# Kernel optimization log

Measured on AMD Instinct MI355X. Metric: run time of the kernel, lower is better.

Reference implementation:

```python
import jax, jax.numpy as jnp
import numpy as np

C_P = 1004.0
R_EARTH = 6371000.0
R_GAS = 287.0
OMEGA_E = 7.292e-05
B, K, H, W = 1, 8, 361, 720
KK = 5   # kernel basis size
D = 5    # neighborhood width in lat and lon (radius 2)
NS = K * 4 + 1
FCH = K * 4
NU = 2.0e5  # diffusion coefficient


def _ch(k, kind):
    return k * 4 + kind


def disco_gather(x, psi, quad):
    # DISCO sparse neighborhood aggregation on the sphere.
    # x: (B,C,H,W); psi: (KK,2,H,D,D) lat-dependent filter basis (2 directional comps)
    # returns (B,C,KK,2,H,W)
    Bx, C, Hx, Wx = x.shape
    Kk, nc, _, Dlat, Dlon = psi.shape
    r = Dlat // 2
    lat = np.clip(np.arange(Hx)[:, None] + np.arange(Dlat)[None, :] - r, 0, Hx - 1)
    out = jnp.zeros((Bx, C, Kk, nc, Hx, Wx), x.dtype)
    for dl in range(Dlat):
        li = lat[:, dl]
        xg = x[:, :, li, :] * quad[li][None, None, :, None]  # quadrature-weighted gather
        for dw in range(Dlon):
            xs = jnp.roll(xg, -(dw - r), axis=-1)  # circular in longitude
            out = out + psi[:, :, :, dl, dw][None, None, :, :, :, None] * xs[:, :, None, None, :, :]
    return out


def setup_inputs():
    key = jax.random.key(0)
    k1, k2, k3 = jax.random.split(key, 3)
    uv = jax.random.normal(k1, (B, K, H, W, 2), jnp.float32)
    T = jax.random.normal(k2, (B, K, H, W), jnp.float32)
    q = jax.random.normal(k3, (B, K, H, W), jnp.float32)
    rng = np.random.RandomState(0)
    psi = ((rng.rand(KK, 2, H, D, D) - 0.5) / (D * D)).astype(np.float32)
    colat = np.linspace(0.0, np.pi, H)
    quad = (np.sin(colat) * np.pi / (H - 1)).astype(np.float32)
    f_cor = (2.0 * OMEGA_E * np.sin(np.pi / 2.0 - colat)).astype(np.float32)
    p = np.array([1e5 * np.exp(-k * np.log(10.0) / (K - 1)) for k in range(K)], np.float32)
    lpr = np.log(p[:-1] / p[1:])
    p_low = np.concatenate([p[:1], 0.5 * (p[:-1] + p[1:])])
    p_up = np.concatenate([0.5 * (p[:-1] + p[1:]), [0.0]])
    dp = (p_low - p_up).astype(np.float32)
    # physics-encoded weights (module freezes all params and sets them analytically)
    W_ss_blk = np.zeros((NS, NS, KK), np.float32)
    W_vs_blk = np.zeros((NS, K, KK, 2), np.float32)
    for k in range(K):
        W_vs_blk[_ch(k, 2), k, :, 0] = 1.0 / R_EARTH  # zeta (curl)
        W_vs_blk[_ch(k, 3), k, :, 1] = 1.0 / R_EARTH  # div
    W_sv_blk = np.zeros((K, NS, KK, 2), np.float32)
    for ko in range(K):
        for ki in range(ko):
            W_sv_blk[ko, _ch(ki, 0), :, 1] = -R_GAS * lpr[ki] / R_EARTH  # PGF
        W_sv_blk[ko, _ch(ko, 1), :, 1] = -1.0 / R_EARTH  # -grad KE
    W_vv_blk = np.zeros((K, K, KK, 2), np.float32)
    W_vs2_blk = np.zeros((NS, K, KK, 2), np.float32)
    W_pw_ss = np.zeros((NS, NS), np.float32)
    W_pw_ss[FCH, FCH] = 1.0
    W_svp = np.zeros((NS, K, 2), np.float32)
    for k in range(K):
        W_svp[_ch(k, 2), k, 1] = 1.0
    W_svp[FCH, :, 1] = -1.0
    W_pw_vv = np.zeros((K, K), np.float32)
    W_ss_adv = np.zeros((2 * K, 2 * K, KK), np.float32)
    W_vs_adv = np.zeros((2 * K, K, KK, 2), np.float32)
    W_vs2_adv = np.zeros((2 * K, K, KK, 2), np.float32)
    for k in range(K):
        W_vs2_adv[k, k, :, 1] = -1.0 / R_EARTH      # -V.grad T
        W_vs2_adv[K + k, k, :, 1] = -1.0 / R_EARTH  # -V.grad q
    W_sv_grad = np.zeros((1, 1, KK, 2), np.float32)
    W_sv_grad[0, 0, :, 1] = 1.0 / R_EARTH
    W_vs_div = np.zeros((1, 1, KK, 2), np.float32)
    W_vs_div[0, 0, :, 1] = 1.0 / R_EARTH
    j = jnp.asarray
    return dict(uv=uv, T=T, q=q, psi=j(psi), quad=j(quad), f_cor=j(f_cor), p_levels=j(p), delta_p=j(dp),
                W_ss_blk=j(W_ss_blk), W_vs_blk=j(W_vs_blk), W_sv_blk=j(W_sv_blk), W_vv_blk=j(W_vv_blk),
                W_vs2_blk=j(W_vs2_blk), W_pw_ss=j(W_pw_ss), W_svp=j(W_svp), W_pw_vv=j(W_pw_vv),
                W_ss_adv=j(W_ss_adv), W_vs_adv=j(W_vs_adv), W_vs2_adv=j(W_vs2_adv),
                W_sv_grad=j(W_sv_grad), W_vs_div=j(W_vs_div))


def _forward(uv, T, q, psi, quad, f_cor, p_levels, delta_p, W_ss_blk, W_vs_blk, W_sv_blk, W_vv_blk,
             W_vs2_blk, W_pw_ss, W_svp, W_pw_vv, W_ss_adv, W_vs_adv, W_vs2_adv, W_sv_grad, W_vs_div):
    Bx, Kx, Hx, Wx = T.shape
    ke = 0.5 * (uv[..., 0] ** 2 + uv[..., 1] ** 2)
    zeros = jnp.zeros_like(T)
    per = jnp.stack([T, ke, zeros, zeros], axis=2).reshape(Bx, Kx * 4, Hx, Wx)
    f_field = jnp.broadcast_to(f_cor[None, None, :, None], (Bx, 1, Hx, Wx))
    x_s = jnp.concatenate([per, f_field], axis=1)  # (B, 4K+1, H, W)
    # ---- Block 1: VectorDiscoBlock ----
    Gs = disco_gather(x_s, psi, quad)               # (B,NS,KK,2,H,W)
    Ga = disco_gather(uv[..., 0], psi, quad)
    Gb = disco_gather(uv[..., 1], psi, quad)
    Gdir = jnp.stack([Ga[:, :, :, 0], Gb[:, :, :, 1]], axis=3)  # curl/div pairing
    Giso = jnp.stack([Ga[:, :, :, 0], Gb[:, :, :, 0]], axis=3)
    ys_c = jnp.einsum('oik,bikhw->bohw', W_ss_blk, Gs[:, :, :, 0])
    ys_c = ys_c + jnp.einsum('oikc,bikchw->bohw', W_vs_blk, Gdir)
    ys_c = ys_c + jnp.einsum('oikc,bokchw,bihwc->bohw', W_vs2_blk, Gs, uv)
    yv_c = jnp.einsum('oikc,bikchw->bohwc', W_sv_blk, Gs)
    yv_c = yv_c + jnp.einsum('oikc,bikchw->bohwc', W_vv_blk, Giso)
    s_feat = ys_c + jnp.einsum('oi,bihw->bohw', W_pw_ss, x_s)
    coef0 = jnp.einsum('ij,bihw->bjhw', W_svp[:, :, 0], s_feat)
    coef1 = jnp.einsum('ij,bihw->bjhw', W_svp[:, :, 1], s_feat)
    cross = jnp.stack([-uv[..., 1], uv[..., 0]], axis=-1)  # k-hat x V
    sv = coef0[..., None] * uv + coef1[..., None] * cross
    y_v = uv + yv_c + sv + jnp.einsum('oi,bihwc->bohwc', W_pw_vv, uv)
    y_s = s_feat
    duv_dt = y_v - uv
    # omega from divergence (upward pressure integral)
    div = y_s[:, :Kx * 4].reshape(Bx, Kx, 4, Hx, Wx)[:, :, 3]
    cum = jnp.cumsum(div * delta_p[None, :, None, None], axis=1)
    omega = 0.5 * (jnp.concatenate([jnp.zeros_like(cum[:, :1]), cum[:, :-1]], axis=1) + cum)
    # ---- adv_conv (W_vs2 pathway): -V.grad(T), -V.grad(q) ----
    tq = jnp.concatenate([T, q], axis=1)
    Gtq = disco_gather(tq, psi, quad)
    dTq = jnp.einsum('oik,bikhw->bohw', W_ss_adv, Gtq[:, :, :, 0])
    dTq = dTq + jnp.einsum('oikc,bikchw->bohw', W_vs_adv, Gdir)
    dTq = dTq + jnp.einsum('oikc,bokchw,bihwc->bohw', W_vs2_adv, Gtq, uv)
    dT_dt = dTq[:, :Kx]
    dq_dt = dTq[:, Kx:]
    # dT/dp central differences
    p = p_levels
    inter = (T[:, 2:] - T[:, :-2]) / (p[2:] - p[:-2])[None, :, None, None]
    first = (T[:, 1:2] - T[:, 0:1]) / (p[1] - p[0])
    last = (T[:, -1:] - T[:, -2:-1]) / (p[-1] - p[-2])
    dTdp = jnp.concatenate([first, inter, last], axis=1)
    pk = p[None, :, None, None]
    dT_dt = dT_dt + omega * (R_GAS / C_P * T / pk - dTdp)
    # ---- diffusion: nu * div(grad(s)) via grad_conv/div_conv ----
    def lap(s):
        sf = s.reshape(Bx * Kx, 1, Hx, Wx)
        Gsf = disco_gather(sf, psi, quad)
        g = jnp.einsum('oikc,bikchw->bohwc', W_sv_grad, Gsf)  # (BK,1,H,W,2)
        Gga = disco_gather(g[..., 0], psi, quad)
        Ggb = disco_gather(g[..., 1], psi, quad)
        Gd = jnp.stack([Gga[:, :, :, 0], Ggb[:, :, :, 1]], axis=3)
        return jnp.einsum('oikc,bikchw->bohw', W_vs_div, Gd).reshape(Bx, Kx, Hx, Wx)
    dT_dt = dT_dt + NU * lap(T)
    dq_dt = dq_dt + NU * lap(q)
    duv_dt = duv_dt + NU * jnp.stack([lap(uv[..., 0]), lap(uv[..., 1])], axis=-1)
    return duv_dt, dT_dt, dq_dt


def reference(uv, T, q, psi, quad, f_cor, p_levels, delta_p, W_ss_blk, W_vs_blk, W_sv_blk, W_vv_blk,
              W_vs2_blk, W_pw_ss, W_svp, W_pw_vv, W_ss_adv, W_vs_adv, W_vs2_adv, W_sv_grad, W_vs_div):
    return _forward(uv, T, q, psi, quad, f_cor, p_levels, delta_p, W_ss_blk, W_vs_blk, W_sv_blk,
                    W_vv_blk, W_vs2_blk, W_pw_ss, W_svp, W_pw_vv, W_ss_adv, W_vs_adv, W_vs2_adv,
                    W_sv_grad, W_vs_div)
```

## Files before the change

### kernel.cpp

```cpp
#include <hip/hip_runtime.h>


constexpr int Kz = 8, Hh = 361, Ww = 720;
constexpr int HW = Hh * Ww;
constexpr int OFF_DT = Kz * HW * 2;
constexpr int OFF_DQ = OFF_DT + Kz * HW;

constexpr int TH = 16, TW = 64;
constexpr int SH = TH + 8, SW4 = TW + 8;
constexpr int EH = TH + 4, EW4 = TW + 4;
constexpr int SW4P = 73;
constexpr int EW4P = 69;

__device__ __forceinline__ int clipH(int x) {
  return x < 0 ? 0 : (x > Hh - 1 ? Hh - 1 : x);
}

#define FMA4(acc, s, v)                                                        \
  do {                                                                         \
    acc.x = fmaf((s), (v).x, acc.x);                                           \
    acc.y = fmaf((s), (v).y, acc.y);                                           \
    acc.z = fmaf((s), (v).z, acc.z);                                           \
    acc.w = fmaf((s), (v).w, acc.w);                                           \
  } while (0)

#define ROWV(acc, a, b, c, d, e)                                               \
  do {                                                                         \
    FMA4(acc, wq0, a); FMA4(acc, wq1, b); FMA4(acc, wq2, c);                   \
    FMA4(acc, wq3, d); FMA4(acc, wq4, e);                                      \
  } while (0)

#define ROW5S(acc, q0, q1, q2, q3, q4, a, b, c, d, e)                          \
  acc = fmaf(q0, a, fmaf(q1, b, fmaf(q2, c, fmaf(q3, d, fmaf(q4, e, acc)))))

__global__ __launch_bounds__(256, 2) void pe_pass1(
    const float2* __restrict__ uv,
    const float*  __restrict__ Tg,
    const float*  __restrict__ qg,
    const float*  __restrict__ psi,
    const float*  __restrict__ quad,
    const float*  __restrict__ f_cor,
    const float*  __restrict__ delta_p,
    float* __restrict__ out,
    float2* __restrict__ ws)
{
  __shared__ float4 S4[SH][SW4P];
  __shared__ float4 d1S[EH][EW4P];
  __shared__ __align__(16) float uSh[SH][SW4];
  __shared__ __align__(16) float keSh[SH][SW4];
  __shared__ float P1L[EH][25];
  __shared__ float P0L[TH][25];
  __shared__ float quadA[SH];

  const int tid = threadIdx.x;
  const int tx = tid & 15;
  const int ty = tid >> 4;
  const int w0 = blockIdx.x * TW;
  const int h0 = blockIdx.y * TH;
  const int k  = blockIdx.z;

  if (tid < SH) quadA[tid] = quad[clipH(h0 + tid - 4)];
  for (int idx = tid; idx < EH * 25; idx += 256) {
    int ee = idx / 25, t = idx - ee * 25;
    int p = clipH(h0 + ee - 2);
    float s = 0.f;
    #pragma unroll
    for (int kk = 0; kk < 5; ++kk)
      s += psi[kk * (2 * Hh * 25) + Hh * 25 + p * 25 + t];
    P1L[ee][t] = s;
  }
  for (int idx = tid; idx < TH * 25; idx += 256) {
    int r = idx / 25, t = idx - r * 25;
    int p = clipH(h0 + r);
    float s = 0.f;
    #pragma unroll
    for (int kk = 0; kk < 5; ++kk)
      s += psi[kk * (2 * Hh * 25) + p * 25 + t];
    P0L[r][t] = s;
  }

  for (int idx = tid; idx < SH * SW4; idx += 256) {
    int rr = idx / SW4, cc = idx - rr * SW4;
    int pr = clipH(h0 + rr - 4);
    int pc = w0 + cc - 4;
    pc = pc < 0 ? pc + Ww : (pc >= Ww ? pc - Ww : pc);
    int g = (k * Hh + pr) * Ww + pc;
    float2 uvv = uv[g];
    float tv = Tg[g], qv_ = qg[g];
    S4[rr][cc] = make_float4(uvv.x, uvv.y, tv, qv_);
    if (cc >= 2) {
      uSh[rr][cc - 2]  = uvv.x;
      keSh[rr][cc - 2] = 0.5f * (uvv.x * uvv.x + uvv.y * uvv.y);
    }
  }
  __syncthreads();

  for (int idx = tid; idx < EH * (EW4 / 4); idx += 256) {
    int ee = idx / (EW4 / 4), gc = idx - ee * (EW4 / 4);
    int cb = gc * 4;
    int p = clipH(h0 + ee - 2);
    float4 a0 = {0,0,0,0}, a1 = {0,0,0,0}, a2 = {0,0,0,0}, a3 = {0,0,0,0};
    #pragma unroll
    for (int dl = 0; dl < 5; ++dl) {
      int sp = clipH(p + dl - 2);
      int rr = sp - h0 + 4;
      float qv = quadA[rr];
      const float4* row = &S4[rr][cb];
      float4 g0 = row[0], g1 = row[1], g2 = row[2], g3 = row[3];
      float4 g4 = row[4], g5 = row[5], g6 = row[6], g7 = row[7];
      const float* wr = &P1L[ee][dl * 5];
      float wq0 = qv * wr[0], wq1 = qv * wr[1], wq2 = qv * wr[2];
      float wq3 = qv * wr[3], wq4 = qv * wr[4];
      ROWV(a0, g0, g1, g2, g3, g4);
      ROWV(a1, g1, g2, g3, g4, g5);
      ROWV(a2, g2, g3, g4, g5, g6);
      ROWV(a3, g3, g4, g5, g6, g7);
    }
    d1S[ee][cb + 0] = a0; d1S[ee][cb + 1] = a1;
    d1S[ee][cb + 2] = a2; d1S[ee][cb + 3] = a3;
  }
  __syncthreads();

  const int h = h0 + ty;
  const int hc = h < Hh ? h : (Hh - 1);
  const int wbase = w0 + tx * 4;
  const float f = f_cor[hc];
  const float invR = (float)(1.0 / 6371000.0);
  const float cL = 200000.0f * invR * invR;

  float4 lp0 = {0,0,0,0}, lp1 = {0,0,0,0}, lp2 = {0,0,0,0}, lp3 = {0,0,0,0};
  float du0 = 0.f, du1 = 0.f, du2 = 0.f, du3 = 0.f;
  float dk0 = 0.f, dk1 = 0.f, dk2 = 0.f, dk3 = 0.f;
  #pragma unroll
  for (int dl = 0; dl < 5; ++dl) {
    int sp = clipH(hc + dl - 2);
    int er = sp - h0 + 2;
    int rr = er + 2;
    float qv = quadA[rr];
    {
      const float4* row = &d1S[er][tx * 4];
      float4 g0 = row[0], g1 = row[1], g2 = row[2], g3 = row[3];
      float4 g4 = row[4], g5 = row[5], g6 = row[6], g7 = row[7];
      const float* wr = &P1L[ty + 2][dl * 5];
      float wq0 = qv * wr[0], wq1 = qv * wr[1], wq2 = qv * wr[2];
      float wq3 = qv * wr[3], wq4 = qv * wr[4];
      ROWV(lp0, g0, g1, g2, g3, g4);
      ROWV(lp1, g1, g2, g3, g4, g5);
      ROWV(lp2, g2, g3, g4, g5, g6);
      ROWV(lp3, g3, g4, g5, g6, g7);
    }
    {
      float4 A = *(const float4*)&uSh[rr][tx * 4];
      float4 B = *(const float4*)&uSh[rr][tx * 4 + 4];
      const float* w0r = &P0L[ty][dl * 5];
      float q0 = qv * w0r[0], q1 = qv * w0r[1], q2 = qv * w0r[2];
      float q3 = qv * w0r[3], q4 = qv * w0r[4];
      ROW5S(du0, q0, q1, q2, q3, q4, A.x, A.y, A.z, A.w, B.x);
      ROW5S(du1, q0, q1, q2, q3, q4, A.y, A.z, A.w, B.x, B.y);
      ROW5S(du2, q0, q1, q2, q3, q4, A.z, A.w, B.x, B.y, B.z);
      ROW5S(du3, q0, q1, q2, q3, q4, A.w, B.x, B.y, B.z, B.w);
    }
    {
      float4 A = *(const float4*)&keSh[rr][tx * 4];
      float4 B = *(const float4*)&keSh[rr][tx * 4 + 4];
      const float* w1r = &P1L[ty + 2][dl * 5];
      float q0 = qv * w1r[0], q1 = qv * w1r[1], q2 = qv * w1r[2];
      float q3 = qv * w1r[3], q4 = qv * w1r[4];
      ROW5S(dk0, q0, q1, q2, q3, q4, A.x, A.y, A.z, A.w, B.x);
      ROW5S(dk1, q0, q1, q2, q3, q4, A.y, A.z, A.w, B.x, B.y);
      ROW5S(dk2, q0, q1, q2, q3, q4, A.z, A.w, B.x, B.y, B.z);
      ROW5S(dk3, q0, q1, q2, q3, q4, A.w, B.x, B.y, B.z, B.w);
    }
  }

  if (h < Hh && wbase < Ww) {
    const float dpk = delta_p[k];
    float4 duvA, duvB, dTv, dqv, wsA, wsB;
    {
      float4 d1c = d1S[ty + 2][tx * 4 + 2];
      float4 ctr = S4[ty + 4][tx * 4 + 4];
      float coef1 = fmaf(du0, invR, -f);
      duvA.x = fmaf(-coef1, ctr.y, cL * lp0.x);
      duvA.y = fmaf(coef1, ctr.x, -invR * dk0) + cL * lp0.y;
      dTv.x = -(invR * d1c.z) * ctr.y + cL * lp0.z;
      dqv.x = fmaf(-(invR * d1c.w), ctr.y, cL * lp0.w);
      wsA.x = invR * d1c.y * dpk; wsA.y = d1c.z;
    }
    {
      float4 d1c = d1S[ty + 2][tx * 4 + 3];
      float4 ctr = S4[ty + 4][tx * 4 + 5];
      float coef1 = fmaf(du1, invR, -f);
      duvA.z = fmaf(-coef1, ctr.y, cL * lp1.x);
      duvA.w = fmaf(coef1, ctr.x, -invR * dk1) + cL * lp1.y;
      dTv.y = -(invR * d1c.z) * ctr.y + cL * lp1.z;
      dqv.y = fmaf(-(invR * d1c.w), ctr.y, cL * lp1.w);
      wsA.z = invR * d1c.y * dpk; wsA.w = d1c.z;
    }
    {
      float4 d1c = d1S[ty + 2][tx * 4 + 4];
      float4 ctr = S4[ty + 4][tx * 4 + 6];
      float coef1 = fmaf(du2, invR, -f);
      duvB.x = fmaf(-coef1, ctr.y, cL * lp2.x);
      duvB.y = fmaf(coef1, ctr.x, -invR * dk2) + cL * lp2.y;
      dTv.z = -(invR * d1c.z) * ctr.y + cL * lp2.z;
      dqv.z = fmaf(-(invR * d1c.w), ctr.y, cL * lp2.w);
      wsB.x = invR * d1c.y * dpk; wsB.y = d1c.z;
    }
    {
      float4 d1c = d1S[ty + 2][tx * 4 + 5];
      float4 ctr = S4[ty + 4][tx * 4 + 7];
      float coef1 = fmaf(du3, invR, -f);
      duvB.z = fmaf(-coef1, ctr.y, cL * lp3.x);
      duvB.w = fmaf(coef1, ctr.x, -invR * dk3) + cL * lp3.y;
      dTv.w = -(invR * d1c.z) * ctr.y + cL * lp3.z;
      dqv.w = fmaf(-(invR * d1c.w), ctr.y, cL * lp3.w);
      wsB.z = invR * d1c.y * dpk; wsB.w = d1c.z;
    }
    const int gidx = (k * Hh + h) * Ww + wbase;
    float4* o4 = (float4*)out;
    o4[gidx >> 1] = duvA;
    o4[(gidx >> 1) + 1] = duvB;
    *(float4*)&out[OFF_DT + gidx] = dTv;
    *(float4*)&out[OFF_DQ + gidx] = dqv;
    float4* w4 = (float4*)ws;
    w4[gidx >> 1] = wsA;
    w4[(gidx >> 1) + 1] = wsB;
  }
}

__global__ __launch_bounds__(256) void pe_pass2(
    const float* __restrict__ Tg,
    const float* __restrict__ p_levels,
    const float2* __restrict__ ws,
    float* __restrict__ out)
{
  int hw = blockIdx.x * 256 + threadIdx.x;
  if (hw >= HW) return;
  const float invR = (float)(1.0 / 6371000.0);
  const float RCP = (float)(287.0 / 1004.0);

  float pl[Kz];
  #pragma unroll
  for (int k = 0; k < Kz; ++k) pl[k] = p_levels[k];

  float cum = 0.f, sumT = 0.f;
  float Tm = 0.f, Tc = Tg[hw];
  float2* o2 = (float2*)out;

  #pragma unroll
  for (int k = 0; k < Kz; ++k) {
    float Tp = (k < Kz - 1) ? Tg[(k + 1) * HW + hw] : 0.f;
    float2 wsv = ws[k * HW + hw];
    float omega = fmaf(0.5f, wsv.x, cum);
    cum += wsv.x;

    float dTdp;
    if (k == 0)            dTdp = (Tp - Tc) / (pl[1] - pl[0]);
    else if (k == Kz - 1)  dTdp = (Tc - Tm) / (pl[Kz - 1] - pl[Kz - 2]);
    else                   dTdp = (Tp - Tm) / (pl[k + 1] - pl[k - 1]);

    float fac = (RCP * Tc) / pl[k] - dTdp;
    out[OFF_DT + k * HW + hw] += omega * fac;

    float2 o = o2[k * HW + hw];
    o.y += sumT;
    o2[k * HW + hw] = o;

    if (k < Kz - 1) {
      float lpr = logf(pl[k] / pl[k + 1]);
      sumT = fmaf(-287.0f * lpr * invR, wsv.y, sumT);
    }
    Tm = Tc; Tc = Tp;
  }
}

constexpr int FTH = 16, FTW = 16;
constexpr int FSH = FTH + 8, FSW = FTW + 8;
constexpr int FEH = FTH + 4, FEW = FTW + 4;
constexpr int FSWp = FSW + 1, FEWp = FEW + 1;

__global__ __launch_bounds__(256) void pe_step(
    const float2* __restrict__ uv,
    const float*  __restrict__ Tg,
    const float*  __restrict__ qg,
    const float*  __restrict__ psi,
    const float*  __restrict__ quad,
    const float*  __restrict__ f_cor,
    const float*  __restrict__ p_levels,
    const float*  __restrict__ delta_p,
    float* __restrict__ out)
{
  __shared__ float uS[FSH][FSWp], vS[FSH][FSWp], TS[FSH][FSWp], qS[FSH][FSWp];
  __shared__ float keS[FEH][FEWp];
  __shared__ float d1uS[FEH][FEWp], d1vS[FEH][FEWp], d1TS[FEH][FEWp], d1qS[FEH][FEWp];
  __shared__ float P1L[FEH][25];
  __shared__ float P0L[FTH][25];
  __shared__ float quadA[FSH];
  __shared__ float pl[8], dps[8];

  const int tid = threadIdx.x;
  const int tx = tid & (FTW - 1);
  const int ty = tid >> 4;
  const int w0 = blockIdx.x * FTW;
  const int h0 = blockIdx.y * FTH;

  if (tid < FSH) quadA[tid] = quad[clipH(h0 + tid - 4)];
  if (tid < 8) { pl[tid] = p_levels[tid]; dps[tid] = delta_p[tid]; }
  for (int idx = tid; idx < FEH * 25; idx += 256) {
    int ee = idx / 25, t = idx - ee * 25;
    int p = clipH(h0 + ee - 2);
    float s = 0.f;
    #pragma unroll
    for (int kk = 0; kk < 5; ++kk)
      s += psi[kk * (2 * Hh * 25) + Hh * 25 + p * 25 + t];
    P1L[ee][t] = s;
  }
  for (int idx = tid; idx < FTH * 25; idx += 256) {
    int r = idx / 25, t = idx - r * 25;
    int p = clipH(h0 + r);
    float s = 0.f;
    #pragma unroll
    for (int kk = 0; kk < 5; ++kk)
      s += psi[kk * (2 * Hh * 25) + p * 25 + t];
    P0L[r][t] = s;
  }
  __syncthreads();

  const int h = h0 + ty;
  const bool act = h < Hh;
  const int hc = act ? h : (Hh - 1);
  const int w = w0 + tx;
  const float f = f_cor[hc];
  const float invR = (float)(1.0 / 6371000.0);
  const float cL = 200000.0f * invR * invR;
  const float RCP = (float)(287.0 / 1004.0);

  float cum = 0.f;
  float sumT = 0.f;

  #pragma unroll 1
  for (int k = 0; k < Kz; ++k) {
    __syncthreads();
    for (int idx = tid; idx < FSH * FSW; idx += 256) {
      int rr = idx / FSW, cc = idx - rr * FSW;
      int pr = clipH(h0 + rr - 4);
      int pc = w0 + cc - 4;
      pc = pc < 0 ? pc + Ww : (pc >= Ww ? pc - Ww : pc);
      int g = (k * Hh + pr) * Ww + pc;
      float2 uvv = uv[g];
      uS[rr][cc] = uvv.x; vS[rr][cc] = uvv.y;
      TS[rr][cc] = Tg[g]; qS[rr][cc] = qg[g];
    }
    __syncthreads();
    for (int idx = tid; idx < FEH * FEW; idx += 256) {
      int ee = idx / FEW, ec = idx - ee * FEW;
      float su = uS[ee + 2][ec + 2], sv = vS[ee + 2][ec + 2];
      keS[ee][ec] = 0.5f * (su * su + sv * sv);
    }
    for (int idx = tid; idx < FEH * FEW; idx += 256) {
      int ee = idx / FEW, ec = idx - ee * FEW;
      int p = clipH(h0 + ee - 2);
      float au = 0.f, av = 0.f, aT = 0.f, aq = 0.f;
      #pragma unroll
      for (int dl = 0; dl < 5; ++dl) {
        int sp = clipH(p + dl - 2);
        int rr = sp - h0 + 4;
        float qv = quadA[rr];
        float ru = 0.f, rv = 0.f, rT = 0.f, rq = 0.f;
        #pragma unroll
        for (int dw = 0; dw < 5; ++dw) {
          float wgt = P1L[ee][dl * 5 + dw];
          ru = fmaf(wgt, uS[rr][ec + dw], ru);
          rv = fmaf(wgt, vS[rr][ec + dw], rv);
          rT = fmaf(wgt, TS[rr][ec + dw], rT);
          rq = fmaf(wgt, qS[rr][ec + dw], rq);
        }
        au = fmaf(qv, ru, au); av = fmaf(qv, rv, av);
        aT = fmaf(qv, rT, aT); aq = fmaf(qv, rq, aq);
      }
      d1uS[ee][ec] = au; d1vS[ee][ec] = av;
      d1TS[ee][ec] = aT; d1qS[ee][ec] = aq;
    }
    __syncthreads();

    float d0u = 0.f, d1ke = 0.f;
    #pragma unroll
    for (int dl = 0; dl < 5; ++dl) {
      int sp = clipH(hc + dl - 2);
      int rr = sp - h0 + 4;
      int er = sp - h0 + 2;
      float qv = quadA[rr];
      float r0 = 0.f, rk = 0.f;
      #pragma unroll
      for (int dw = 0; dw < 5; ++dw) {
        r0 = fmaf(P0L[ty][dl * 5 + dw], uS[rr][tx + 2 + dw], r0);
        rk = fmaf(P1L[ty + 2][dl * 5 + dw], keS[er][tx + dw], rk);
      }
      d0u = fmaf(qv, r0, d0u);
      d1ke = fmaf(qv, rk, d1ke);
    }

    float lapu = 0.f, lapv = 0.f, lapT = 0.f, lapq = 0.f;
    #pragma unroll
    for (int dl = 0; dl < 5; ++dl) {
      int sp = clipH(hc + dl - 2);
      int er = sp - h0 + 2;
      float qv = quadA[er + 2];
      float ru = 0.f, rv = 0.f, rT = 0.f, rq = 0.f;
      #pragma unroll
      for (int dw = 0; dw < 5; ++dw) {
        float wgt = P1L[ty + 2][dl * 5 + dw];
        ru = fmaf(wgt, d1uS[er][tx + dw], ru);
        rv = fmaf(wgt, d1vS[er][tx + dw], rv);
        rT = fmaf(wgt, d1TS[er][tx + dw], rT);
        rq = fmaf(wgt, d1qS[er][tx + dw], rq);
      }
      lapu = fmaf(qv, ru, lapu); lapv = fmaf(qv, rv, lapv);
      lapT = fmaf(qv, rT, lapT); lapq = fmaf(qv, rq, lapq);
    }

    float d1T_c = d1TS[ty + 2][tx + 2];
    float d1v_c = d1vS[ty + 2][tx + 2];
    float d1q_c = d1qS[ty + 2][tx + 2];
    float uc = uS[ty + 4][tx + 4], vc = vS[ty + 4][tx + 4];
    float Tc = TS[ty + 4][tx + 4];

    float coef1 = fmaf(d0u, invR, -f);
    float duv0 = fmaf(-coef1, vc, cL * lapu);
    float yv1 = fmaf(-invR, d1ke, sumT);
    float duv1 = fmaf(coef1, uc, yv1) + cL * lapv;

    float div = invR * d1v_c;
    float dpk = dps[k];
    float omega = fmaf(0.5f * div, dpk, cum);
    cum = fmaf(div, dpk, cum);

    int gidx = (k * Hh + hc) * Ww + w;
    float dTdp;
    if (k == 0) {
      float Tp = Tg[gidx + HW];
      dTdp = (Tp - Tc) / (pl[1] - pl[0]);
    } else if (k == Kz - 1) {
      float Tm = Tg[gidx - HW];
      dTdp = (Tc - Tm) / (pl[Kz - 1] - pl[Kz - 2]);
    } else {
      float Tp = Tg[gidx + HW];
      float Tm = Tg[gidx - HW];
      dTdp = (Tp - Tm) / (pl[k + 1] - pl[k - 1]);
    }
    float adv = -(invR * d1T_c) * vc;
    float dT = adv + omega * ((RCP * Tc) / pl[k] - dTdp) + cL * lapT;
    float dq = fmaf(-(invR * d1q_c), vc, cL * lapq);

    if (act) {
      ((float2*)out)[(k * Hh + h) * Ww + w] = make_float2(duv0, duv1);
      out[OFF_DT + gidx] = dT;
      out[OFF_DQ + gidx] = dq;
    }

    if (k < Kz - 1) {
      float lpr = logf(pl[k] / pl[k + 1]);
      float wTk = (float)(-287.0 * (double)lpr / 6371000.0);
      sumT = fmaf(wTk, d1T_c, sumT);
    }
  }
}

extern "C" void kernel_launch(void* const* d_in, const int* in_sizes, int n_in,
                              void* d_out, int out_size, void* d_ws, size_t ws_size,
                              hipStream_t stream) {
  (void)in_sizes; (void)n_in; (void)out_size;
  const float2* uv   = (const float2*)d_in[0];
  const float*  T    = (const float*) d_in[1];
  const float*  q    = (const float*) d_in[2];
  const float*  psi  = (const float*) d_in[3];
  const float*  quad = (const float*) d_in[4];
  const float*  fc   = (const float*) d_in[5];
  const float*  pl   = (const float*) d_in[6];
  const float*  dp   = (const float*) d_in[7];

  const size_t ws_need = (size_t)Kz * HW * sizeof(float2);
  if (ws_size >= ws_need) {
    dim3 g1((Ww + TW - 1) / TW, (Hh + TH - 1) / TH, Kz);
    hipLaunchKernelGGL(pe_pass1, g1, dim3(256), 0, stream,
                       uv, T, q, psi, quad, fc, dp, (float*)d_out, (float2*)d_ws);
    dim3 g2((HW + 255) / 256);
    hipLaunchKernelGGL(pe_pass2, g2, dim3(256), 0, stream,
                       T, pl, (const float2*)d_ws, (float*)d_out);
  } else {
    dim3 grid(Ww / FTW, (Hh + FTH - 1) / FTH);
    hipLaunchKernelGGL(pe_step, grid, dim3(256), 0, stream,
                       uv, T, q, psi, quad, fc, pl, dp, (float*)d_out);
  }
}
```

Measured before the change: 80.73 us.

## Shrink pass1 LDS footprint, fold quadrature into weights, vectorize pass2

Pass1 drops the separate u and kinetic-energy shared arrays and the quad array. It reads u and recomputes KE from the packed S4 tile, and premultiplies the psi weight tables by the quadrature factor. Occupancy is raised to 3 blocks per SM, and the first-stage thread mapping is transposed. Pass2 now processes two pixels per thread with float2/float4 accesses and reciprocal multiplies in place of divides. The smaller LDS footprint and fewer multiplies cost some redundant KE arithmetic and tighter register limits.

```diff
diff --git a/kernel.cpp b/kernel.cpp
--- a/kernel.cpp
+++ b/kernel.cpp
@@ -33,7 +33,7 @@
 #define ROW5S(acc, q0, q1, q2, q3, q4, a, b, c, d, e)                          \
   acc = fmaf(q0, a, fmaf(q1, b, fmaf(q2, c, fmaf(q3, d, fmaf(q4, e, acc)))))
 
-__global__ __launch_bounds__(256, 2) void pe_pass1(
+__global__ __launch_bounds__(256, 3) void pe_pass1(
     const float2* __restrict__ uv,
     const float*  __restrict__ Tg,
     const float*  __restrict__ qg,
@@ -46,11 +46,8 @@
 {
   __shared__ float4 S4[SH][SW4P];
   __shared__ float4 d1S[EH][EW4P];
-  __shared__ __align__(16) float uSh[SH][SW4];
-  __shared__ __align__(16) float keSh[SH][SW4];
-  __shared__ float P1L[EH][25];
-  __shared__ float P0L[TH][25];
-  __shared__ float quadA[SH];
+  __shared__ float P1q[EH][25];
+  __shared__ float P0q[TH][25];
 
   const int tid = threadIdx.x;
   const int tx = tid & 15;
@@ -59,24 +56,25 @@
   const int h0 = blockIdx.y * TH;
   const int k  = blockIdx.z;
 
-  if (tid < SH) quadA[tid] = quad[clipH(h0 + tid - 4)];
   for (int idx = tid; idx < EH * 25; idx += 256) {
     int ee = idx / 25, t = idx - ee * 25;
     int p = clipH(h0 + ee - 2);
+    int dl = t / 5;
     float s = 0.f;
     #pragma unroll
     for (int kk = 0; kk < 5; ++kk)
       s += psi[kk * (2 * Hh * 25) + Hh * 25 + p * 25 + t];
-    P1L[ee][t] = s;
+    P1q[ee][t] = s * quad[clipH(p + dl - 2)];
   }
   for (int idx = tid; idx < TH * 25; idx += 256) {
     int r = idx / 25, t = idx - r * 25;
     int p = clipH(h0 + r);
+    int dl = t / 5;
     float s = 0.f;
     #pragma unroll
     for (int kk = 0; kk < 5; ++kk)
       s += psi[kk * (2 * Hh * 25) + p * 25 + t];
-    P0L[r][t] = s;
+    P0q[r][t] = s * quad[clipH(p + dl - 2)];
   }
 
   for (int idx = tid; idx < SH * SW4; idx += 256) {
@@ -86,17 +84,13 @@
     pc = pc < 0 ? pc + Ww : (pc >= Ww ? pc - Ww : pc);
     int g = (k * Hh + pr) * Ww + pc;
     float2 uvv = uv[g];
-    float tv = Tg[g], qv_ = qg[g];
-    S4[rr][cc] = make_float4(uvv.x, uvv.y, tv, qv_);
-    if (cc >= 2) {
-      uSh[rr][cc - 2]  = uvv.x;
-      keSh[rr][cc - 2] = 0.5f * (uvv.x * uvv.x + uvv.y * uvv.y);
-    }
+    S4[rr][cc] = make_float4(uvv.x, uvv.y, Tg[g], qg[g]);
   }
   __syncthreads();
 
   for (int idx = tid; idx < EH * (EW4 / 4); idx += 256) {
-    int ee = idx / (EW4 / 4), gc = idx - ee * (EW4 / 4);
+    int ee = idx % EH;
+    int gc = idx / EH;
     int cb = gc * 4;
     int p = clipH(h0 + ee - 2);
     float4 a0 = {0,0,0,0}, a1 = {0,0,0,0}, a2 = {0,0,0,0}, a3 = {0,0,0,0};
@@ -104,13 +98,11 @@
     for (int dl = 0; dl < 5; ++dl) {
       int sp = clipH(p + dl - 2);
       int rr = sp - h0 + 4;
-      float qv = quadA[rr];
       const float4* row = &S4[rr][cb];
       float4 g0 = row[0], g1 = row[1], g2 = row[2], g3 = row[3];
       float4 g4 = row[4], g5 = row[5], g6 = row[6], g7 = row[7];
-      const float* wr = &P1L[ee][dl * 5];
-      float wq0 = qv * wr[0], wq1 = qv * wr[1], wq2 = qv * wr[2];
-      float wq3 = qv * wr[3], wq4 = qv * wr[4];
+      const float* wr = &P1q[ee][dl * 5];
+      float wq0 = wr[0], wq1 = wr[1], wq2 = wr[2], wq3 = wr[3], wq4 = wr[4];
       ROWV(a0, g0, g1, g2, g3, g4);
       ROWV(a1, g1, g2, g3, g4, g5);
       ROWV(a2, g2, g3, g4, g5, g6);
@@ -126,6 +118,7 @@
   const int wbase = w0 + tx * 4;
   const float f = f_cor[hc];
   const float invR = (float)(1.0 / 6371000.0);
+  const float halfInvR = 0.5f * invR;
   const float cL = 200000.0f * invR * invR;
 
   float4 lp0 = {0,0,0,0}, lp1 = {0,0,0,0}, lp2 = {0,0,0,0}, lp3 = {0,0,0,0};
@@ -136,40 +129,39 @@
     int sp = clipH(hc + dl - 2);
     int er = sp - h0 + 2;
     int rr = er + 2;
-    float qv = quadA[rr];
+    const float* wr = &P1q[ty + 2][dl * 5];
+    float wq0 = wr[0], wq1 = wr[1], wq2 = wr[2], wq3 = wr[3], wq4 = wr[4];
     {
       const float4* row = &d1S[er][tx * 4];
       float4 g0 = row[0], g1 = row[1], g2 = row[2], g3 = row[3];
       float4 g4 = row[4], g5 = row[5], g6 = row[6], g7 = row[7];
-      const float* wr = &P1L[ty + 2][dl * 5];
-      float wq0 = qv * wr[0], wq1 = qv * wr[1], wq2 = qv * wr[2];
-      float wq3 = qv * wr[3], wq4 = qv * wr[4];
       ROWV(lp0, g0, g1, g2, g3, g4);
       ROWV(lp1, g1, g2, g3, g4, g5);
       ROWV(lp2, g2, g3, g4, g5, g6);
       ROWV(lp3, g3, g4, g5, g6, g7);
     }
     {
-      float4 A = *(const float4*)&uSh[rr][tx * 4];
-      float4 B = *(const float4*)&uSh[rr][tx * 4 + 4];
-      const float* w0r = &P0L[ty][dl * 5];
-      float q0 = qv * w0r[0], q1 = qv * w0r[1], q2 = qv * w0r[2];
-      float q3 = qv * w0r[3], q4 = qv * w0r[4];
-      ROW5S(du0, q0, q1, q2, q3, q4, A.x, A.y, A.z, A.w, B.x);
-      ROW5S(du1, q0, q1, q2, q3, q4, A.y, A.z, A.w, B.x, B.y);
-      ROW5S(du2, q0, q1, q2, q3, q4, A.z, A.w, B.x, B.y, B.z);
-      ROW5S(du3, q0, q1, q2, q3, q4, A.w, B.x, B.y, B.z, B.w);
-    }
-    {
-      float4 A = *(const float4*)&keSh[rr][tx * 4];
-      float4 B = *(const float4*)&keSh[rr][tx * 4 + 4];
-      const float* w1r = &P1L[ty + 2][dl * 5];
-      float q0 = qv * w1r[0], q1 = qv * w1r[1], q2 = qv * w1r[2];
-      float q3 = qv * w1r[3], q4 = qv * w1r[4];
-      ROW5S(dk0, q0, q1, q2, q3, q4, A.x, A.y, A.z, A.w, B.x);
-      ROW5S(dk1, q0, q1, q2, q3, q4, A.y, A.z, A.w, B.x, B.y);
-      ROW5S(dk2, q0, q1, q2, q3, q4, A.z, A.w, B.x, B.y, B.z);
-      ROW5S(dk3, q0, q1, q2, q3, q4, A.w, B.x, B.y, B.z, B.w);
+      const float4* srow = &S4[rr][tx * 4 + 2];
+      float4 s0 = srow[0], s1 = srow[1], s2 = srow[2], s3 = srow[3];
+      float4 s4 = srow[4], s5 = srow[5], s6 = srow[6], s7 = srow[7];
+      float k0 = fmaf(s0.y, s0.y, s0.x * s0.x);
+      float k1 = fmaf(s1.y, s1.y, s1.x * s1.x);
+      float k2 = fmaf(s2.y, s2.y, s2.x * s2.x);
+      float k3 = fmaf(s3.y, s3.y, s3.x * s3.x);
+      float k4 = fmaf(s4.y, s4.y, s4.x * s4.x);
+      float k5 = fmaf(s5.y, s5.y, s5.x * s5.x);
+      float k6 = fmaf(s6.y, s6.y, s6.x * s6.x);
+      float k7 = fmaf(s7.y, s7.y, s7.x * s7.x);
+      ROW5S(dk0, wq0, wq1, wq2, wq3, wq4, k0, k1, k2, k3, k4);
+      ROW5S(dk1, wq0, wq1, wq2, wq3, wq4, k1, k2, k3, k4, k5);
+      ROW5S(dk2, wq0, wq1, wq2, wq3, wq4, k2, k3, k4, k5, k6);
+      ROW5S(dk3, wq0, wq1, wq2, wq3, wq4, k3, k4, k5, k6, k7);
+      const float* w0r = &P0q[ty][dl * 5];
+      float q0 = w0r[0], q1 = w0r[1], q2 = w0r[2], q3 = w0r[3], q4 = w0r[4];
+      ROW5S(du0, q0, q1, q2, q3, q4, s0.x, s1.x, s2.x, s3.x, s4.x);
+      ROW5S(du1, q0, q1, q2, q3, q4, s1.x, s2.x, s3.x, s4.x, s5.x);
+      ROW5S(du2, q0, q1, q2, q3, q4, s2.x, s3.x, s4.x, s5.x, s6.x);
+      ROW5S(du3, q0, q1, q2, q3, q4, s3.x, s4.x, s5.x, s6.x, s7.x);
     }
   }
 
@@ -181,7 +173,7 @@
       float4 ctr = S4[ty + 4][tx * 4 + 4];
       float coef1 = fmaf(du0, invR, -f);
       duvA.x = fmaf(-coef1, ctr.y, cL * lp0.x);
-      duvA.y = fmaf(coef1, ctr.x, -invR * dk0) + cL * lp0.y;
+      duvA.y = fmaf(coef1, ctr.x, -halfInvR * dk0) + cL * lp0.y;
       dTv.x = -(invR * d1c.z) * ctr.y + cL * lp0.z;
       dqv.x = fmaf(-(invR * d1c.w), ctr.y, cL * lp0.w);
       wsA.x = invR * d1c.y * dpk; wsA.y = d1c.z;
@@ -191,7 +183,7 @@
       float4 ctr = S4[ty + 4][tx * 4 + 5];
       float coef1 = fmaf(du1, invR, -f);
       duvA.z = fmaf(-coef1, ctr.y, cL * lp1.x);
-      duvA.w = fmaf(coef1, ctr.x, -invR * dk1) + cL * lp1.y;
+      duvA.w = fmaf(coef1, ctr.x, -halfInvR * dk1) + cL * lp1.y;
       dTv.y = -(invR * d1c.z) * ctr.y + cL * lp1.z;
       dqv.y = fmaf(-(invR * d1c.w), ctr.y, cL * lp1.w);
       wsA.z = invR * d1c.y * dpk; wsA.w = d1c.z;
@@ -201,7 +193,7 @@
       float4 ctr = S4[ty + 4][tx * 4 + 6];
       float coef1 = fmaf(du2, invR, -f);
       duvB.x = fmaf(-coef1, ctr.y, cL * lp2.x);
-      duvB.y = fmaf(coef1, ctr.x, -invR * dk2) + cL * lp2.y;
+      duvB.y = fmaf(coef1, ctr.x, -halfInvR * dk2) + cL * lp2.y;
       dTv.z = -(invR * d1c.z) * ctr.y + cL * lp2.z;
       dqv.z = fmaf(-(invR * d1c.w), ctr.y, cL * lp2.w);
       wsB.x = invR * d1c.y * dpk; wsB.y = d1c.z;
@@ -211,7 +203,7 @@
       float4 ctr = S4[ty + 4][tx * 4 + 7];
       float coef1 = fmaf(du3, invR, -f);
       duvB.z = fmaf(-coef1, ctr.y, cL * lp3.x);
-      duvB.w = fmaf(coef1, ctr.x, -invR * dk3) + cL * lp3.y;
+      duvB.w = fmaf(coef1, ctr.x, -halfInvR * dk3) + cL * lp3.y;
       dTv.w = -(invR * d1c.z) * ctr.y + cL * lp3.z;
       dqv.w = fmaf(-(invR * d1c.w), ctr.y, cL * lp3.w);
       wsB.z = invR * d1c.y * dpk; wsB.w = d1c.z;
@@ -234,8 +226,8 @@
     const float2* __restrict__ ws,
     float* __restrict__ out)
 {
-  int hw = blockIdx.x * 256 + threadIdx.x;
-  if (hw >= HW) return;
+  int i2 = blockIdx.x * 256 + threadIdx.x;
+  if (i2 >= HW / 2) return;
   const float invR = (float)(1.0 / 6371000.0);
   const float RCP = (float)(287.0 / 1004.0);
 
@@ -243,32 +235,46 @@
   #pragma unroll
   for (int k = 0; k < Kz; ++k) pl[k] = p_levels[k];
 
-  float cum = 0.f, sumT = 0.f;
-  float Tm = 0.f, Tc = Tg[hw];
-  float2* o2 = (float2*)out;
+  const float2* T2 = (const float2*)Tg;
+  const float4* ws4 = (const float4*)ws;
+  float4* o4 = (float4*)out;
+  float2* dT2 = (float2*)(out + OFF_DT);
+
+  float2 cum = {0.f, 0.f}, sumT = {0.f, 0.f};
+  float2 Tm = {0.f, 0.f}, Tc = T2[i2];
 
   #pragma unroll
   for (int k = 0; k < Kz; ++k) {
-    float Tp = (k < Kz - 1) ? Tg[(k + 1) * HW + hw] : 0.f;
-    float2 wsv = ws[k * HW + hw];
-    float omega = fmaf(0.5f, wsv.x, cum);
-    cum += wsv.x;
-
-    float dTdp;
-    if (k == 0)            dTdp = (Tp - Tc) / (pl[1] - pl[0]);
-    else if (k == Kz - 1)  dTdp = (Tc - Tm) / (pl[Kz - 1] - pl[Kz - 2]);
-    else                   dTdp = (Tp - Tm) / (pl[k + 1] - pl[k - 1]);
-
-    float fac = (RCP * Tc) / pl[k] - dTdp;
-    out[OFF_DT + k * HW + hw] += omega * fac;
-
-    float2 o = o2[k * HW + hw];
-    o.y += sumT;
-    o2[k * HW + hw] = o;
+    float2 Tp = (k < Kz - 1) ? T2[(k + 1) * (HW / 2) + i2] : make_float2(0.f, 0.f);
+    float4 wsv = ws4[k * (HW / 2) + i2];
+    float om0 = fmaf(0.5f, wsv.x, cum.x); cum.x += wsv.x;
+    float om1 = fmaf(0.5f, wsv.z, cum.y); cum.y += wsv.z;
+
+    float dTdp0, dTdp1;
+    if (k == 0) {
+      float idp = 1.f / (pl[1] - pl[0]);
+      dTdp0 = (Tp.x - Tc.x) * idp; dTdp1 = (Tp.y - Tc.y) * idp;
+    } else if (k == Kz - 1) {
+      float idp = 1.f / (pl[Kz - 1] - pl[Kz - 2]);
+      dTdp0 = (Tc.x - Tm.x) * idp; dTdp1 = (Tc.y - Tm.y) * idp;
+    } else {
+      float idp = 1.f / (pl[k + 1] - pl[k - 1]);
+      dTdp0 = (Tp.x - Tm.x) * idp; dTdp1 = (Tp.y - Tm.y) * idp;
+    }
+    float iplk = RCP / pl[k];
+    float2 dt = dT2[k * (HW / 2) + i2];
+    dt.x += om0 * (iplk * Tc.x - dTdp0);
+    dt.y += om1 * (iplk * Tc.y - dTdp1);
+    dT2[k * (HW / 2) + i2] = dt;
+
+    float4 o = o4[k * (HW / 2) + i2];
+    o.y += sumT.x; o.w += sumT.y;
+    o4[k * (HW / 2) + i2] = o;
 
     if (k < Kz - 1) {
-      float lpr = logf(pl[k] / pl[k + 1]);
-      sumT = fmaf(-287.0f * lpr * invR, wsv.y, sumT);
+      float c = -287.0f * logf(pl[k] / pl[k + 1]) * invR;
+      sumT.x = fmaf(c, wsv.y, sumT.x);
+      sumT.y = fmaf(c, wsv.w, sumT.y);
     }
     Tm = Tc; Tc = Tp;
   }
@@ -484,7 +490,7 @@
     dim3 g1((Ww + TW - 1) / TW, (Hh + TH - 1) / TH, Kz);
     hipLaunchKernelGGL(pe_pass1, g1, dim3(256), 0, stream,
                        uv, T, q, psi, quad, fc, dp, (float*)d_out, (float2*)d_ws);
-    dim3 g2((HW + 255) / 256);
+    dim3 g2((HW / 2 + 255) / 256);
     hipLaunchKernelGGL(pe_pass2, g2, dim3(256), 0, stream,
                        T, pl, (const float2*)d_ws, (float*)d_out);
   } else {
```

Measured after the change: 79.43 us. Within noise of the previous version (-1.6%).
